# Kernel optimization log

Measured on AMD Instinct MI355X. Metric: run time of the kernel, lower is better.

## Reference

```python
import jax, jax.numpy as jnp
import numpy as np

B, T, D, L, H = 4096, 200, 128, 64, 128  # n_traj, time steps, input_dim, latent_dim, n_units


def _lin(key, fan_in, fan_out):
    s = 1.0 / np.sqrt(fan_in)
    kw, kb = jax.random.split(key)
    w = jax.random.uniform(kw, (fan_in, fan_out), jnp.float32, -s, s)
    b = jax.random.uniform(kb, (fan_out,), jnp.float32, -s, s)
    return w, b


def setup_inputs() -> dict:
    key = jax.random.key(0)
    ks = jax.random.split(key, 8)
    data = jax.random.normal(ks[0], (B, T, D), jnp.float32)
    time_steps = jax.random.uniform(ks[1], (T,), jnp.float32)
    cin = 2 * L + D
    ug_w1, ug_b1 = _lin(ks[2], cin, H)
    ug_w2, ug_b2 = _lin(ks[3], H, L)
    rg_w1, rg_b1 = _lin(ks[4], cin, H)
    rg_w2, rg_b2 = _lin(ks[5], H, L)
    ns_w1, ns_b1 = _lin(ks[6], cin, H)
    ns_w2, ns_b2 = _lin(ks[7], H, 2 * L)
    return dict(data=data, time_steps=time_steps,
                ug_w1=ug_w1, ug_b1=ug_b1, ug_w2=ug_w2, ug_b2=ug_b2,
                rg_w1=rg_w1, rg_b1=rg_b1, rg_w2=rg_w2, rg_b2=rg_b2,
                ns_w1=ns_w1, ns_b1=ns_b1, ns_w2=ns_w2, ns_b2=ns_b2)


def reference(data, time_steps,
              ug_w1, ug_b1, ug_w2, ug_b2,
              rg_w1, rg_b1, rg_w2, rg_b2,
              ns_w1, ns_b1, ns_w2, ns_b2):
    # GRUUnit (latent-ODE style): gates are 2-layer MLPs (Tanh hidden) over
    # concat([y_mean, y_logvar, x]); update/reset end in Sigmoid, new_state
    # net emits 2L (mean, |std|).
    def step(carry, x):  # x: [B, D]
        y, s = carry  # each [B, L]
        h = jnp.concatenate([y, s, x], axis=-1)  # [B, 2L+D]
        u = jax.nn.sigmoid(jnp.tanh(h @ ug_w1 + ug_b1) @ ug_w2 + ug_b2)
        r = jax.nn.sigmoid(jnp.tanh(h @ rg_w1 + rg_b1) @ rg_w2 + rg_b2)
        hc = jnp.concatenate([y * r, s * r, x], axis=-1)
        ns = jnp.tanh(hc @ ns_w1 + ns_b1) @ ns_w2 + ns_b2  # [B, 2L]
        new_mean = ns[:, :L]
        new_std = jnp.abs(ns[:, L:])
        y2 = (1.0 - u) * new_mean + u * y
        s2 = (1.0 - u) * new_std + u * s
        return (y2, s2), None

    y0 = jnp.zeros((data.shape[0], L), data.dtype)
    s0 = jnp.zeros((data.shape[0], L), data.dtype)
    xs = jnp.transpose(data, (1, 0, 2))  # [T, B, D]; scan over time
    (yT, sT), _ = jax.lax.scan(step, (y0, s0), xs)
    return yT, sT
```

## Files before the change

kernel.cpp:

```cpp
#include <hip/hip_runtime.h>
#include <hip/hip_bf16.h>


#define NB 4096
#define NT 200
#define ND 128
#define HS 528
#define TS 272

typedef __bf16 bf16;
typedef __attribute__((ext_vector_type(8))) __bf16 bf16x8;
typedef __attribute__((ext_vector_type(4))) __bf16 bf16x4;
typedef __attribute__((ext_vector_type(4))) float f32x4;

#define BAR() asm volatile("s_waitcnt lgkmcnt(0)\n\ts_barrier" ::: "memory")

__device__ __forceinline__ f32x4 mfma16(bf16x8 a, bf16x8 b, f32x4 c){
    return __builtin_amdgcn_mfma_f32_16x16x32_bf16(a, b, c, 0, 0, 0);
}
__device__ __forceinline__ float fast_tanh(float x){
    float e = __expf(2.f * x);
    return 1.f - 2.f * __builtin_amdgcn_rcpf(e + 1.f);
}
__device__ __forceinline__ float fast_sigmoid(float x){
    return __builtin_amdgcn_rcpf(1.f + __expf(-x));
}
__device__ __forceinline__ bf16x4 tanh4(f32x4 a){
    bf16x4 o;
    o[0] = (bf16)fast_tanh(a[0]);
    o[1] = (bf16)fast_tanh(a[1]);
    o[2] = (bf16)fast_tanh(a[2]);
    o[3] = (bf16)fast_tanh(a[3]);
    return o;
}
__device__ __forceinline__ f32x4 bias4(const float* b, int f){
    f32x4 r; r[0] = b[f]; r[1] = b[f+1]; r[2] = b[f+2]; r[3] = b[f+3]; return r;
}

__global__ __launch_bounds__(512, 2)
void vae_rnn(const float* __restrict__ data,
             const float* __restrict__ ug_w1, const float* __restrict__ ug_b1,
             const float* __restrict__ ug_w2, const float* __restrict__ ug_b2,
             const float* __restrict__ rg_w1, const float* __restrict__ rg_b1,
             const float* __restrict__ rg_w2, const float* __restrict__ rg_b2,
             const float* __restrict__ ns_w1, const float* __restrict__ ns_b1,
             const float* __restrict__ ns_w2, const float* __restrict__ ns_b2,
             float* __restrict__ out)
{
    __shared__ __align__(16) char h_lds [16 * HS];
    __shared__ __align__(16) char t_lds [16 * HS];
    __shared__ __align__(16) char tn_lds[16 * TS];
    __shared__ float u_lds [16][68];
    __shared__ float ys_lds[16][132];

    const int tid  = threadIdx.x;
    const int wave = tid >> 6;
    const int lane = tid & 63;
    const int lq   = lane >> 4;
    const int lc   = lane & 15;
    const int row0 = blockIdx.x * 16;

    const int pr = tid >> 4;
    const int pc = tid & 15;
    const float* xsrc = data + (size_t)(row0 + pr) * (NT * ND) + pc * 8;

    for (int i = tid; i < 16*132; i += 512) (&ys_lds[0][0])[i] = 0.f;
    if (tid < 256){
        bf16x8 z = {};
        *(bf16x8*)(h_lds + pr*HS + pc*16) = z;
        float4 a0 = *(const float4*)xsrc;
        float4 a1 = *(const float4*)(xsrc + 4);
        bf16x8 xv = { (bf16)a0.x,(bf16)a0.y,(bf16)a0.z,(bf16)a0.w,
                      (bf16)a1.x,(bf16)a1.y,(bf16)a1.z,(bf16)a1.w };
        *(bf16x8*)(h_lds + pr*HS + 256 + pc*16) = xv;
    }
    __syncthreads();

    if (wave < 4){
        const int g  = wave;
        const bool UROLE = (g < 2);
        const float* W1 = UROLE ? ug_w1 : rg_w1;
        const float* B1 = UROLE ? ug_b1 : rg_b1;
        const float* W2 = UROLE ? ug_w2 : rg_w2;
        const float* B2 = UROLE ? ug_b2 : rg_b2;
        const int f1 = (g & 1) * 64;
        const int f2 = (g & 1) * 32;

        bf16x8 wA[32]; f32x4 bA[4];
        #pragma unroll
        for (int j = 0; j < 4; ++j){
            int n = f1 + j*16 + lc;
            bA[j] = bias4(B1, f1 + j*16 + lq*4);
            #pragma unroll
            for (int kt = 0; kt < 8; ++kt){
                bf16x8 f;
                #pragma unroll
                for (int e = 0; e < 8; ++e) f[e] = (bf16)W1[(kt*32 + lq*8 + e)*128 + n];
                wA[kt*4 + j] = f;
            }
        }
        bf16x8 wB[8]; f32x4 bB[2];
        #pragma unroll
        for (int j = 0; j < 2; ++j){
            int n = f2 + j*16 + lc;
            bB[j] = bias4(B2, f2 + j*16 + lq*4);
            #pragma unroll
            for (int kt = 0; kt < 4; ++kt){
                bf16x8 f;
                #pragma unroll
                for (int e = 0; e < 8; ++e) f[e] = (bf16)W2[(kt*32 + lq*8 + e)*64 + n];
                wB[kt*2 + j] = f;
            }
        }

        const char* h_rd  = h_lds + lc*HS + lq*16;
        char*       t_wr  = t_lds + lc*HS + g*128 + lq*8;
        const char* t_rd  = t_lds + lc*HS + lq*16 + (UROLE ? 0 : 256);
        char*       hc_wr = h_lds + lc*HS + f2*2 + lq*8;
        char*       x_wr  = h_lds + pr*HS + 256 + pc*16;
        const int   rc    = f2 + lq*4;

        #pragma unroll 1
        for (int t = 0; t < NT; ++t){
            int tn1 = (t + 1 < NT) ? (t + 1) : (NT - 1);
            float4 xa = *(const float4*)(xsrc + (size_t)tn1*ND);
            float4 xb = *(const float4*)(xsrc + (size_t)tn1*ND + 4);

            f32x4 a0 = bA[0], a1 = bA[1], a2 = bA[2], a3 = bA[3];
            #pragma unroll
            for (int kt = 0; kt < 8; ++kt){
                bf16x8 hv = *(const bf16x8*)(h_rd + kt*64);
                a0 = mfma16(wA[kt*4+0], hv, a0);
                a1 = mfma16(wA[kt*4+1], hv, a1);
                a2 = mfma16(wA[kt*4+2], hv, a2);
                a3 = mfma16(wA[kt*4+3], hv, a3);
            }
            *(bf16x4*)(t_wr +  0) = tanh4(a0);
            *(bf16x4*)(t_wr + 32) = tanh4(a1);
            *(bf16x4*)(t_wr + 64) = tanh4(a2);
            *(bf16x4*)(t_wr + 96) = tanh4(a3);
            BAR();

            float4 y0, y1, s0, s1;
            if (!UROLE){
                y0 = *(const float4*)&ys_lds[lc][rc];
                y1 = *(const float4*)&ys_lds[lc][rc + 16];
                s0 = *(const float4*)&ys_lds[lc][64 + rc];
                s1 = *(const float4*)&ys_lds[lc][80 + rc];
            }
            f32x4 b0 = bB[0], b1 = bB[1];
            #pragma unroll
            for (int kt = 0; kt < 4; ++kt){
                bf16x8 tv = *(const bf16x8*)(t_rd + kt*64);
                b0 = mfma16(wB[kt*2+0], tv, b0);
                b1 = mfma16(wB[kt*2+1], tv, b1);
            }
            float g00 = fast_sigmoid(b0[0]), g01 = fast_sigmoid(b0[1]);
            float g02 = fast_sigmoid(b0[2]), g03 = fast_sigmoid(b0[3]);
            float g10 = fast_sigmoid(b1[0]), g11 = fast_sigmoid(b1[1]);
            float g12 = fast_sigmoid(b1[2]), g13 = fast_sigmoid(b1[3]);
            if (UROLE){
                *(float4*)&u_lds[lc][rc]      = make_float4(g00, g01, g02, g03);
                *(float4*)&u_lds[lc][rc + 16] = make_float4(g10, g11, g12, g13);
            } else {
                bf16x4 hy0 = { (bf16)(y0.x*g00), (bf16)(y0.y*g01), (bf16)(y0.z*g02), (bf16)(y0.w*g03) };
                bf16x4 hy1 = { (bf16)(y1.x*g10), (bf16)(y1.y*g11), (bf16)(y1.z*g12), (bf16)(y1.w*g13) };
                bf16x4 hs0 = { (bf16)(s0.x*g00), (bf16)(s0.y*g01), (bf16)(s0.z*g02), (bf16)(s0.w*g03) };
                bf16x4 hs1 = { (bf16)(s1.x*g10), (bf16)(s1.y*g11), (bf16)(s1.z*g12), (bf16)(s1.w*g13) };
                *(bf16x4*)(hc_wr +   0) = hy0;
                *(bf16x4*)(hc_wr +  32) = hy1;
                *(bf16x4*)(hc_wr + 128) = hs0;
                *(bf16x4*)(hc_wr + 160) = hs1;
            }
            BAR();

            BAR();

            {
                bf16x8 xv = { (bf16)xa.x,(bf16)xa.y,(bf16)xa.z,(bf16)xa.w,
                              (bf16)xb.x,(bf16)xb.y,(bf16)xb.z,(bf16)xb.w };
                *(bf16x8*)x_wr = xv;
            }
            BAR();
        }
    } else {
        const int g   = wave - 4;
        const bool STD = (g >= 2);

        bf16x8 wC[16]; f32x4 bC[2];
        #pragma unroll
        for (int j = 0; j < 2; ++j){
            int n = g*32 + j*16 + lc;
            bC[j] = bias4(ns_b1, g*32 + j*16 + lq*4);
            #pragma unroll
            for (int kt = 0; kt < 8; ++kt){
                bf16x8 f;
                #pragma unroll
                for (int e = 0; e < 8; ++e) f[e] = (bf16)ns_w1[(kt*32 + lq*8 + e)*128 + n];
                wC[kt*2 + j] = f;
            }
        }
        bf16x8 wD[8]; f32x4 bD[2];
        #pragma unroll
        for (int j = 0; j < 2; ++j){
            int n = g*32 + j*16 + lc;
            bD[j] = bias4(ns_b2, g*32 + j*16 + lq*4);
            #pragma unroll
            for (int kt = 0; kt < 4; ++kt){
                bf16x8 f;
                #pragma unroll
                for (int e = 0; e < 8; ++e) f[e] = (bf16)ns_w2[(kt*32 + lq*8 + e)*128 + n];
                wD[kt*2 + j] = f;
            }
        }

        const char* x_rd  = h_lds  + lc*HS + 256 + lq*16;
        const char* hc_rd = h_lds  + lc*HS + lq*16;
        char*       tn_wr = tn_lds + lc*TS + g*64 + lq*8;
        const char* tn_rd = tn_lds + lc*TS + lq*16;
        char*       hy_wr = h_lds  + lc*HS + g*64 + lq*8;
        const int   fD = g*32 + lq*4;
        const int   uC = (g & 1)*32 + lq*4;

        f32x4 old0 = {0.f,0.f,0.f,0.f}, old1 = {0.f,0.f,0.f,0.f};

        #pragma unroll 1
        for (int t = 0; t < NT; ++t){
            f32x4 c0 = bC[0], c1 = bC[1];
            #pragma unroll
            for (int kt = 0; kt < 4; ++kt){
                bf16x8 xv = *(const bf16x8*)(x_rd + kt*64);
                c0 = mfma16(wC[(kt+4)*2+0], xv, c0);
                c1 = mfma16(wC[(kt+4)*2+1], xv, c1);
            }
            BAR();

            BAR();

            #pragma unroll
            for (int kt = 0; kt < 4; ++kt){
                bf16x8 hv = *(const bf16x8*)(hc_rd + kt*64);
                c0 = mfma16(wC[kt*2+0], hv, c0);
                c1 = mfma16(wC[kt*2+1], hv, c1);
            }
            *(bf16x4*)(tn_wr +  0) = tanh4(c0);
            *(bf16x4*)(tn_wr + 32) = tanh4(c1);
            BAR();

            float4 u0 = *(const float4*)&u_lds[lc][uC];
            float4 u1 = *(const float4*)&u_lds[lc][uC + 16];
            f32x4 d0 = bD[0], d1 = bD[1];
            #pragma unroll
            for (int kt = 0; kt < 4; ++kt){
                bf16x8 tv = *(const bf16x8*)(tn_rd + kt*64);
                d0 = mfma16(wD[kt*2+0], tv, d0);
                d1 = mfma16(wD[kt*2+1], tv, d1);
            }
            if (STD){
                d0[0] = fabsf(d0[0]); d0[1] = fabsf(d0[1]);
                d0[2] = fabsf(d0[2]); d0[3] = fabsf(d0[3]);
                d1[0] = fabsf(d1[0]); d1[1] = fabsf(d1[1]);
                d1[2] = fabsf(d1[2]); d1[3] = fabsf(d1[3]);
            }
            old0[0] = fmaf(u0.x, old0[0] - d0[0], d0[0]);
            old0[1] = fmaf(u0.y, old0[1] - d0[1], d0[1]);
            old0[2] = fmaf(u0.z, old0[2] - d0[2], d0[2]);
            old0[3] = fmaf(u0.w, old0[3] - d0[3], d0[3]);
            old1[0] = fmaf(u1.x, old1[0] - d1[0], d1[0]);
            old1[1] = fmaf(u1.y, old1[1] - d1[1], d1[1]);
            old1[2] = fmaf(u1.z, old1[2] - d1[2], d1[2]);
            old1[3] = fmaf(u1.w, old1[3] - d1[3], d1[3]);
            *(float4*)&ys_lds[lc][fD]      = make_float4(old0[0], old0[1], old0[2], old0[3]);
            *(float4*)&ys_lds[lc][fD + 16] = make_float4(old1[0], old1[1], old1[2], old1[3]);
            bf16x4 hn0 = { (bf16)old0[0], (bf16)old0[1], (bf16)old0[2], (bf16)old0[3] };
            bf16x4 hn1 = { (bf16)old1[0], (bf16)old1[1], (bf16)old1[2], (bf16)old1[3] };
            *(bf16x4*)(hy_wr +  0) = hn0;
            *(bf16x4*)(hy_wr + 32) = hn1;
            BAR();
        }
    }

    {
        int orow = tid >> 5;
        int ocol = (tid & 31) << 2;
        float4 v = *(const float4*)&ys_lds[orow][ocol];
        size_t gr = (size_t)(row0 + orow);
        if (ocol < 64) *(float4*)&out[gr*64 + ocol] = v;
        else           *(float4*)&out[(size_t)NB*64 + gr*64 + (ocol - 64)] = v;
    }
}

extern "C" void kernel_launch(void* const* d_in, const int* in_sizes, int n_in,
                              void* d_out, int out_size, void* d_ws, size_t ws_size,
                              hipStream_t stream) {
    const float* data  = (const float*)d_in[0];
    const float* ug_w1 = (const float*)d_in[2];
    const float* ug_b1 = (const float*)d_in[3];
    const float* ug_w2 = (const float*)d_in[4];
    const float* ug_b2 = (const float*)d_in[5];
    const float* rg_w1 = (const float*)d_in[6];
    const float* rg_b1 = (const float*)d_in[7];
    const float* rg_w2 = (const float*)d_in[8];
    const float* rg_b2 = (const float*)d_in[9];
    const float* ns_w1 = (const float*)d_in[10];
    const float* ns_b1 = (const float*)d_in[11];
    const float* ns_w2 = (const float*)d_in[12];
    const float* ns_b2 = (const float*)d_in[13];

    hipLaunchKernelGGL(vae_rnn, dim3(NB/16), dim3(512), 0, stream,
                       data, ug_w1, ug_b1, ug_w2, ug_b2,
                       rg_w1, rg_b1, rg_w2, rg_b2,
                       ns_w1, ns_b1, ns_w2, ns_b2,
                       (float*)d_out);
}
```

Baseline: 359.9 us.

## Split block rows into two half-groups and ping-pong gate and state waves

The 16 rows of each block are split into two 8-row halves, each with its own double-buffered LDS state. While the gate waves work on one half, the new-state waves work on the other, so the two wave groups no longer idle waiting on each other's serial stages. The fp32 ys buffer is dropped: state is kept in registers and re-read as bf16 from the h buffer, and final outputs are written straight from registers. This costs extra LDS, more complex barrier phasing and an epilogue step, and reading y/s as bf16 for the reset product may cost some precision. Each MFMA also uses only half of its 16 row slots, so compute efficiency per instruction drops.

```diff
diff --git a/kernel.cpp b/kernel.cpp
--- a/kernel.cpp
+++ b/kernel.cpp
@@ -47,11 +47,10 @@
              const float* __restrict__ ns_w2, const float* __restrict__ ns_b2,
              float* __restrict__ out)
 {
-    __shared__ __align__(16) char h_lds [16 * HS];
-    __shared__ __align__(16) char t_lds [16 * HS];
-    __shared__ __align__(16) char tn_lds[16 * TS];
-    __shared__ float u_lds [16][68];
-    __shared__ float ys_lds[16][132];
+    __shared__ __align__(16) char h_lds [2][16 * HS];
+    __shared__ __align__(16) char t_lds [2][16 * HS];
+    __shared__ __align__(16) char tn_lds[2][16 * TS];
+    __shared__ float u_lds[2][16][68];
 
     const int tid  = threadIdx.x;
     const int wave = tid >> 6;
@@ -60,31 +59,30 @@
     const int lc   = lane & 15;
     const int row0 = blockIdx.x * 16;
 
-    const int pr = tid >> 4;
-    const int pc = tid & 15;
-    const float* xsrc = data + (size_t)(row0 + pr) * (NT * ND) + pc * 8;
-
-    for (int i = tid; i < 16*132; i += 512) (&ys_lds[0][0])[i] = 0.f;
+    for (int i = tid; i < 2*16*HS/16; i += 512){
+        bf16x8 z = {};
+        *(bf16x8*)(&h_lds[0][0] + i*16) = z;
+    }
     if (tid < 256){
-        bf16x8 z = {};
-        *(bf16x8*)(h_lds + pr*HS + pc*16) = z;
-        float4 a0 = *(const float4*)xsrc;
-        float4 a1 = *(const float4*)(xsrc + 4);
+        int sr = tid >> 7, pr0 = (tid >> 4) & 7, pc0 = tid & 15;
+        const float* xs = data + (size_t)(row0 + sr*8 + pr0) * (NT*ND) + pc0*8;
+        float4 a0 = *(const float4*)xs;
+        float4 a1 = *(const float4*)(xs + 4);
         bf16x8 xv = { (bf16)a0.x,(bf16)a0.y,(bf16)a0.z,(bf16)a0.w,
                       (bf16)a1.x,(bf16)a1.y,(bf16)a1.z,(bf16)a1.w };
-        *(bf16x8*)(h_lds + pr*HS + 256 + pc*16) = xv;
+        *(bf16x8*)(&h_lds[sr][0] + pr0*HS + 256 + pc0*16) = xv;
     }
     __syncthreads();
 
     if (wave < 4){
-        const int g  = wave;
-        const bool UROLE = (g < 2);
-        const float* W1 = UROLE ? ug_w1 : rg_w1;
-        const float* B1 = UROLE ? ug_b1 : rg_b1;
-        const float* W2 = UROLE ? ug_w2 : rg_w2;
-        const float* B2 = UROLE ? ug_b2 : rg_b2;
-        const int f1 = (g & 1) * 64;
-        const int f2 = (g & 1) * 32;
+        const int  w  = wave;
+        const bool UR = (w < 2);
+        const int  f1 = (w & 1) * 64;
+        const int  f2 = (w & 1) * 32;
+        const float* W1 = UR ? ug_w1 : rg_w1;
+        const float* B1 = UR ? ug_b1 : rg_b1;
+        const float* W2 = UR ? ug_w2 : rg_w2;
+        const float* B2 = UR ? ug_b2 : rg_b2;
 
         bf16x8 wA[32]; f32x4 bA[4];
         #pragma unroll
@@ -113,78 +111,73 @@
             }
         }
 
-        const char* h_rd  = h_lds + lc*HS + lq*16;
-        char*       t_wr  = t_lds + lc*HS + g*128 + lq*8;
-        const char* t_rd  = t_lds + lc*HS + lq*16 + (UROLE ? 0 : 256);
-        char*       hc_wr = h_lds + lc*HS + f2*2 + lq*8;
-        char*       x_wr  = h_lds + pr*HS + 256 + pc*16;
-        const int   rc    = f2 + lq*4;
+        const int hrd = lc*HS + lq*16;
+        const int twr = lc*HS + w*128 + lq*8;
+        const int trd = lc*HS + lq*16 + (UR ? 0 : 256);
+        const int yso = lc*HS + 2*(f2 + lq*4);
+        const int uco = f2 + lq*4;
 
         #pragma unroll 1
         for (int t = 0; t < NT; ++t){
-            int tn1 = (t + 1 < NT) ? (t + 1) : (NT - 1);
-            float4 xa = *(const float4*)(xsrc + (size_t)tn1*ND);
-            float4 xb = *(const float4*)(xsrc + (size_t)tn1*ND + 4);
-
-            f32x4 a0 = bA[0], a1 = bA[1], a2 = bA[2], a3 = bA[3];
-            #pragma unroll
-            for (int kt = 0; kt < 8; ++kt){
-                bf16x8 hv = *(const bf16x8*)(h_rd + kt*64);
-                a0 = mfma16(wA[kt*4+0], hv, a0);
-                a1 = mfma16(wA[kt*4+1], hv, a1);
-                a2 = mfma16(wA[kt*4+2], hv, a2);
-                a3 = mfma16(wA[kt*4+3], hv, a3);
-            }
-            *(bf16x4*)(t_wr +  0) = tanh4(a0);
-            *(bf16x4*)(t_wr + 32) = tanh4(a1);
-            *(bf16x4*)(t_wr + 64) = tanh4(a2);
-            *(bf16x4*)(t_wr + 96) = tanh4(a3);
-            BAR();
-
-            float4 y0, y1, s0, s1;
-            if (!UROLE){
-                y0 = *(const float4*)&ys_lds[lc][rc];
-                y1 = *(const float4*)&ys_lds[lc][rc + 16];
-                s0 = *(const float4*)&ys_lds[lc][64 + rc];
-                s1 = *(const float4*)&ys_lds[lc][80 + rc];
-            }
-            f32x4 b0 = bB[0], b1 = bB[1];
-            #pragma unroll
-            for (int kt = 0; kt < 4; ++kt){
-                bf16x8 tv = *(const bf16x8*)(t_rd + kt*64);
-                b0 = mfma16(wB[kt*2+0], tv, b0);
-                b1 = mfma16(wB[kt*2+1], tv, b1);
-            }
-            float g00 = fast_sigmoid(b0[0]), g01 = fast_sigmoid(b0[1]);
-            float g02 = fast_sigmoid(b0[2]), g03 = fast_sigmoid(b0[3]);
-            float g10 = fast_sigmoid(b1[0]), g11 = fast_sigmoid(b1[1]);
-            float g12 = fast_sigmoid(b1[2]), g13 = fast_sigmoid(b1[3]);
-            if (UROLE){
-                *(float4*)&u_lds[lc][rc]      = make_float4(g00, g01, g02, g03);
-                *(float4*)&u_lds[lc][rc + 16] = make_float4(g10, g11, g12, g13);
-            } else {
-                bf16x4 hy0 = { (bf16)(y0.x*g00), (bf16)(y0.y*g01), (bf16)(y0.z*g02), (bf16)(y0.w*g03) };
-                bf16x4 hy1 = { (bf16)(y1.x*g10), (bf16)(y1.y*g11), (bf16)(y1.z*g12), (bf16)(y1.w*g13) };
-                bf16x4 hs0 = { (bf16)(s0.x*g00), (bf16)(s0.y*g01), (bf16)(s0.z*g02), (bf16)(s0.w*g03) };
-                bf16x4 hs1 = { (bf16)(s1.x*g10), (bf16)(s1.y*g11), (bf16)(s1.z*g12), (bf16)(s1.w*g13) };
-                *(bf16x4*)(hc_wr +   0) = hy0;
-                *(bf16x4*)(hc_wr +  32) = hy1;
-                *(bf16x4*)(hc_wr + 128) = hs0;
-                *(bf16x4*)(hc_wr + 160) = hs1;
-            }
-            BAR();
-
-            BAR();
-
-            {
-                bf16x8 xv = { (bf16)xa.x,(bf16)xa.y,(bf16)xa.z,(bf16)xa.w,
-                              (bf16)xb.x,(bf16)xb.y,(bf16)xb.z,(bf16)xb.w };
-                *(bf16x8*)x_wr = xv;
-            }
-            BAR();
-        }
+            #pragma unroll
+            for (int ph = 0; ph < 2; ++ph){
+                char* hb = &h_lds[ph][0];
+                char* tb = &t_lds[ph][0];
+                f32x4 a0 = bA[0], a1 = bA[1], a2 = bA[2], a3 = bA[3];
+                #pragma unroll
+                for (int kt = 0; kt < 8; ++kt){
+                    bf16x8 hv = *(const bf16x8*)(hb + hrd + kt*64);
+                    a0 = mfma16(wA[kt*4+0], hv, a0);
+                    a1 = mfma16(wA[kt*4+1], hv, a1);
+                    a2 = mfma16(wA[kt*4+2], hv, a2);
+                    a3 = mfma16(wA[kt*4+3], hv, a3);
+                }
+                *(bf16x4*)(tb + twr +  0) = tanh4(a0);
+                *(bf16x4*)(tb + twr + 32) = tanh4(a1);
+                *(bf16x4*)(tb + twr + 64) = tanh4(a2);
+                *(bf16x4*)(tb + twr + 96) = tanh4(a3);
+                BAR();
+                bf16x4 yb0, yb1, sb0, sb1;
+                if (!UR){
+                    yb0 = *(const bf16x4*)(hb + yso);
+                    yb1 = *(const bf16x4*)(hb + yso + 32);
+                    sb0 = *(const bf16x4*)(hb + yso + 128);
+                    sb1 = *(const bf16x4*)(hb + yso + 160);
+                }
+                f32x4 b0 = bB[0], b1 = bB[1];
+                #pragma unroll
+                for (int kt = 0; kt < 4; ++kt){
+                    bf16x8 tv = *(const bf16x8*)(tb + trd + kt*64);
+                    b0 = mfma16(wB[kt*2+0], tv, b0);
+                    b1 = mfma16(wB[kt*2+1], tv, b1);
+                }
+                float g00 = fast_sigmoid(b0[0]), g01 = fast_sigmoid(b0[1]);
+                float g02 = fast_sigmoid(b0[2]), g03 = fast_sigmoid(b0[3]);
+                float g10 = fast_sigmoid(b1[0]), g11 = fast_sigmoid(b1[1]);
+                float g12 = fast_sigmoid(b1[2]), g13 = fast_sigmoid(b1[3]);
+                if (UR){
+                    *(float4*)&u_lds[ph][lc][uco]      = make_float4(g00,g01,g02,g03);
+                    *(float4*)&u_lds[ph][lc][uco + 16] = make_float4(g10,g11,g12,g13);
+                } else {
+                    bf16x4 hy0 = { (bf16)((float)yb0[0]*g00), (bf16)((float)yb0[1]*g01),
+                                   (bf16)((float)yb0[2]*g02), (bf16)((float)yb0[3]*g03) };
+                    bf16x4 hy1 = { (bf16)((float)yb1[0]*g10), (bf16)((float)yb1[1]*g11),
+                                   (bf16)((float)yb1[2]*g12), (bf16)((float)yb1[3]*g13) };
+                    bf16x4 hs0 = { (bf16)((float)sb0[0]*g00), (bf16)((float)sb0[1]*g01),
+                                   (bf16)((float)sb0[2]*g02), (bf16)((float)sb0[3]*g03) };
+                    bf16x4 hs1 = { (bf16)((float)sb1[0]*g10), (bf16)((float)sb1[1]*g11),
+                                   (bf16)((float)sb1[2]*g12), (bf16)((float)sb1[3]*g13) };
+                    *(bf16x4*)(hb + yso +   0) = hy0;
+                    *(bf16x4*)(hb + yso +  32) = hy1;
+                    *(bf16x4*)(hb + yso + 128) = hs0;
+                    *(bf16x4*)(hb + yso + 160) = hs1;
+                }
+                BAR();
+            }
+        }
+        BAR();
     } else {
-        const int g   = wave - 4;
+        const int  g   = wave - 4;
         const bool STD = (g >= 2);
 
         bf16x8 wC[16]; f32x4 bC[2];
@@ -214,79 +207,129 @@
             }
         }
 
-        const char* x_rd  = h_lds  + lc*HS + 256 + lq*16;
-        const char* hc_rd = h_lds  + lc*HS + lq*16;
-        char*       tn_wr = tn_lds + lc*TS + g*64 + lq*8;
-        const char* tn_rd = tn_lds + lc*TS + lq*16;
-        char*       hy_wr = h_lds  + lc*HS + g*64 + lq*8;
-        const int   fD = g*32 + lq*4;
-        const int   uC = (g & 1)*32 + lq*4;
-
-        f32x4 old0 = {0.f,0.f,0.f,0.f}, old1 = {0.f,0.f,0.f,0.f};
+        const int hrd = lc*HS + lq*16;
+        const int tnw = lc*TS + g*64 + lq*8;
+        const int tnr = lc*TS + lq*16;
+        const int hyw = lc*HS + g*64 + lq*8;
+        const int uco = (g & 1)*32 + lq*4;
+        const bool XW = (g < 2);
+        const int  pr = (tid & 127) >> 4;
+        const int  pc = tid & 15;
+        const float* xsA = data + (size_t)(row0 + pr)     * (NT*ND) + pc*8;
+        const float* xsB = data + (size_t)(row0 + 8 + pr) * (NT*ND) + pc*8;
+        char* xwA = &h_lds[0][0] + pr*HS + 256 + pc*16;
+        char* xwB = &h_lds[1][0] + pr*HS + 256 + pc*16;
+
+        f32x4 st0[2], st1[2];
+        st0[0] = (f32x4){0,0,0,0}; st0[1] = (f32x4){0,0,0,0};
+        st1[0] = (f32x4){0,0,0,0}; st1[1] = (f32x4){0,0,0,0};
 
         #pragma unroll 1
         for (int t = 0; t < NT; ++t){
+            float4 xa0, xa1, xb0, xb1;
+            if (XW){
+                int t1 = (t + 1 < NT) ? (t + 1) : (NT - 1);
+                xa0 = *(const float4*)(xsA + (size_t)t1*ND);
+                xa1 = *(const float4*)(xsA + (size_t)t1*ND + 4);
+                xb0 = *(const float4*)(xsB + (size_t)t*ND);
+                xb1 = *(const float4*)(xsB + (size_t)t*ND + 4);
+            }
+            #pragma unroll
+            for (int ph = 0; ph < 2; ++ph){
+                const int sg = 1 - ph;
+                char* hb  = &h_lds[sg][0];
+                char* tnb = &tn_lds[sg][0];
+                const bool act = (ph == 1) || (t > 0);
+                if (act){
+                    f32x4 c0 = bC[0], c1 = bC[1];
+                    #pragma unroll
+                    for (int kt = 0; kt < 8; ++kt){
+                        bf16x8 hv = *(const bf16x8*)(hb + hrd + kt*64);
+                        c0 = mfma16(wC[kt*2+0], hv, c0);
+                        c1 = mfma16(wC[kt*2+1], hv, c1);
+                    }
+                    *(bf16x4*)(tnb + tnw +  0) = tanh4(c0);
+                    *(bf16x4*)(tnb + tnw + 32) = tanh4(c1);
+                }
+                BAR();
+                if (act){
+                    f32x4 u4a = *(const f32x4*)&u_lds[sg][lc][uco];
+                    f32x4 u4b = *(const f32x4*)&u_lds[sg][lc][uco + 16];
+                    f32x4 d0 = bD[0], d1 = bD[1];
+                    #pragma unroll
+                    for (int kt = 0; kt < 4; ++kt){
+                        bf16x8 tv = *(const bf16x8*)(tnb + tnr + kt*64);
+                        d0 = mfma16(wD[kt*2+0], tv, d0);
+                        d1 = mfma16(wD[kt*2+1], tv, d1);
+                    }
+                    #pragma unroll
+                    for (int i = 0; i < 4; ++i){
+                        float v0 = STD ? fabsf(d0[i]) : d0[i];
+                        float v1 = STD ? fabsf(d1[i]) : d1[i];
+                        st0[sg][i] = fmaf(u4a[i], st0[sg][i] - v0, v0);
+                        st1[sg][i] = fmaf(u4b[i], st1[sg][i] - v1, v1);
+                    }
+                    bf16x4 hn0 = { (bf16)st0[sg][0], (bf16)st0[sg][1],
+                                   (bf16)st0[sg][2], (bf16)st0[sg][3] };
+                    bf16x4 hn1 = { (bf16)st1[sg][0], (bf16)st1[sg][1],
+                                   (bf16)st1[sg][2], (bf16)st1[sg][3] };
+                    *(bf16x4*)(hb + hyw +  0) = hn0;
+                    *(bf16x4*)(hb + hyw + 32) = hn1;
+                }
+                if (XW){
+                    if (ph == 0){
+                        bf16x8 xv = { (bf16)xb0.x,(bf16)xb0.y,(bf16)xb0.z,(bf16)xb0.w,
+                                      (bf16)xb1.x,(bf16)xb1.y,(bf16)xb1.z,(bf16)xb1.w };
+                        *(bf16x8*)xwB = xv;
+                    } else {
+                        bf16x8 xv = { (bf16)xa0.x,(bf16)xa0.y,(bf16)xa0.z,(bf16)xa0.w,
+                                      (bf16)xa1.x,(bf16)xa1.y,(bf16)xa1.z,(bf16)xa1.w };
+                        *(bf16x8*)xwA = xv;
+                    }
+                }
+                BAR();
+            }
+        }
+        {
+            char* hb  = &h_lds[1][0];
+            char* tnb = &tn_lds[1][0];
             f32x4 c0 = bC[0], c1 = bC[1];
             #pragma unroll
-            for (int kt = 0; kt < 4; ++kt){
-                bf16x8 xv = *(const bf16x8*)(x_rd + kt*64);
-                c0 = mfma16(wC[(kt+4)*2+0], xv, c0);
-                c1 = mfma16(wC[(kt+4)*2+1], xv, c1);
-            }
-            BAR();
-
-            BAR();
-
-            #pragma unroll
-            for (int kt = 0; kt < 4; ++kt){
-                bf16x8 hv = *(const bf16x8*)(hc_rd + kt*64);
+            for (int kt = 0; kt < 8; ++kt){
+                bf16x8 hv = *(const bf16x8*)(hb + hrd + kt*64);
                 c0 = mfma16(wC[kt*2+0], hv, c0);
                 c1 = mfma16(wC[kt*2+1], hv, c1);
             }
-            *(bf16x4*)(tn_wr +  0) = tanh4(c0);
-            *(bf16x4*)(tn_wr + 32) = tanh4(c1);
+            *(bf16x4*)(tnb + tnw +  0) = tanh4(c0);
+            *(bf16x4*)(tnb + tnw + 32) = tanh4(c1);
             BAR();
-
-            float4 u0 = *(const float4*)&u_lds[lc][uC];
-            float4 u1 = *(const float4*)&u_lds[lc][uC + 16];
+            f32x4 u4a = *(const f32x4*)&u_lds[1][lc][uco];
+            f32x4 u4b = *(const f32x4*)&u_lds[1][lc][uco + 16];
             f32x4 d0 = bD[0], d1 = bD[1];
             #pragma unroll
             for (int kt = 0; kt < 4; ++kt){
-                bf16x8 tv = *(const bf16x8*)(tn_rd + kt*64);
+                bf16x8 tv = *(const bf16x8*)(tnb + tnr + kt*64);
                 d0 = mfma16(wD[kt*2+0], tv, d0);
                 d1 = mfma16(wD[kt*2+1], tv, d1);
             }
-            if (STD){
-                d0[0] = fabsf(d0[0]); d0[1] = fabsf(d0[1]);
-                d0[2] = fabsf(d0[2]); d0[3] = fabsf(d0[3]);
-                d1[0] = fabsf(d1[0]); d1[1] = fabsf(d1[1]);
-                d1[2] = fabsf(d1[2]); d1[3] = fabsf(d1[3]);
-            }
-            old0[0] = fmaf(u0.x, old0[0] - d0[0], d0[0]);
-            old0[1] = fmaf(u0.y, old0[1] - d0[1], d0[1]);
-            old0[2] = fmaf(u0.z, old0[2] - d0[2], d0[2]);
-            old0[3] = fmaf(u0.w, old0[3] - d0[3], d0[3]);
-            old1[0] = fmaf(u1.x, old1[0] - d1[0], d1[0]);
-            old1[1] = fmaf(u1.y, old1[1] - d1[1], d1[1]);
-            old1[2] = fmaf(u1.z, old1[2] - d1[2], d1[2]);
-            old1[3] = fmaf(u1.w, old1[3] - d1[3], d1[3]);
-            *(float4*)&ys_lds[lc][fD]      = make_float4(old0[0], old0[1], old0[2], old0[3]);
-            *(float4*)&ys_lds[lc][fD + 16] = make_float4(old1[0], old1[1], old1[2], old1[3]);
-            bf16x4 hn0 = { (bf16)old0[0], (bf16)old0[1], (bf16)old0[2], (bf16)old0[3] };
-            bf16x4 hn1 = { (bf16)old1[0], (bf16)old1[1], (bf16)old1[2], (bf16)old1[3] };
-            *(bf16x4*)(hy_wr +  0) = hn0;
-            *(bf16x4*)(hy_wr + 32) = hn1;
-            BAR();
-        }
-    }
-
-    {
-        int orow = tid >> 5;
-        int ocol = (tid & 31) << 2;
-        float4 v = *(const float4*)&ys_lds[orow][ocol];
-        size_t gr = (size_t)(row0 + orow);
-        if (ocol < 64) *(float4*)&out[gr*64 + ocol] = v;
-        else           *(float4*)&out[(size_t)NB*64 + gr*64 + (ocol - 64)] = v;
+            #pragma unroll
+            for (int i = 0; i < 4; ++i){
+                float v0 = STD ? fabsf(d0[i]) : d0[i];
+                float v1 = STD ? fabsf(d1[i]) : d1[i];
+                st0[1][i] = fmaf(u4a[i], st0[1][i] - v0, v0);
+                st1[1][i] = fmaf(u4b[i], st1[1][i] - v1, v1);
+            }
+        }
+        if (lc < 8){
+            size_t grA = (size_t)(row0 + lc);
+            size_t grB = (size_t)(row0 + 8 + lc);
+            int f = (g & 1)*32 + lq*4;
+            float* base = STD ? (out + (size_t)NB*64) : out;
+            *(float4*)&base[grA*64 + f]      = make_float4(st0[0][0],st0[0][1],st0[0][2],st0[0][3]);
+            *(float4*)&base[grA*64 + f + 16] = make_float4(st1[0][0],st1[0][1],st1[0][2],st1[0][3]);
+            *(float4*)&base[grB*64 + f]      = make_float4(st0[1][0],st0[1][1],st0[1][2],st0[1][3]);
+            *(float4*)&base[grB*64 + f + 16] = make_float4(st1[1][0],st1[1][1],st1[1][2],st1[1][3]);
+        }
     }
 }
 
```

After: 485.2 us. 34.8% more time.
